# Kernel optimization log

Hardware: AMD Instinct MI355X
Metric: run time of the kernel (lower is better)

The kernel has to match this reference:

```python
import jax, jax.numpy as jnp
import numpy as np

N_HEAD = 16
ROPE_CACHE = 2500  # Rotary module caches tables of length 2500
NEG_INF = -1e30


def _rope_tables(head_dim):
    inv_freq = 1.0 / (10000.0 ** (jnp.arange(0, head_dim, 2, dtype=jnp.float32) / head_dim))
    t = jnp.arange(ROPE_CACHE, dtype=jnp.float32)
    freqs = t[:, None] * inv_freq[None, :]            # (2500, head_dim//2)
    emb = jnp.concatenate([freqs, freqs], axis=-1)    # (2500, head_dim)
    return jnp.cos(emb), jnp.sin(emb)


def _rotate_half(x):
    h = x.shape[-1] // 2
    return jnp.concatenate([-x[..., h:], x[..., :h]], axis=-1)


def setup_inputs() -> dict:
    key = jax.random.key(0)
    ks = jax.random.split(key, 8)
    B, S, D = 2, 2048, 1024
    H = N_HEAD
    hd = D // H
    return {
        "qx": jax.random.normal(ks[0], (B, S, D), jnp.float32),
        "kvx": jax.random.normal(ks[1], (B, S, D), jnp.float32),
        "k_cache": jnp.zeros((B, H, S, hd), jnp.float32),
        "v_cache": jnp.zeros((B, H, S, hd), jnp.float32),
        "Wq": jax.random.normal(ks[2], (D, D), jnp.float32) * 0.02,
        "bq": jnp.zeros((D,), jnp.float32),
        "Wk": jax.random.normal(ks[3], (D, D), jnp.float32) * 0.02,
        "Wv": jax.random.normal(ks[4], (D, D), jnp.float32) * 0.02,
        "bv": jnp.zeros((D,), jnp.float32),
        "Wo": jax.random.normal(ks[5], (D, D), jnp.float32) * 0.02,
        "bo": jnp.zeros((D,), jnp.float32),
        "q_positions": jnp.arange(S, dtype=jnp.int32),
        "kv_positions": jnp.arange(S, dtype=jnp.int32),
    }


def reference(qx, kvx, k_cache, v_cache, Wq, bq, Wk, Wv, bv, Wo, bo, q_positions, kv_positions):
    B, Sq, D = qx.shape
    H = N_HEAD
    hd = D // H
    Skv = kvx.shape[1]
    cos, sin = _rope_tables(hd)
    # sqrt_qk_scale = sqrt(1) = 1, folded out.

    def rope(x, pos):  # x: (B, S, H, hd)
        c = cos[pos][None, :, None, :]
        s = sin[pos][None, :, None, :]
        return x * c + _rotate_half(x) * s

    # projections (torch Linear: y = x @ W.T + b; key has no bias)
    q = (qx @ Wq.T + bq).reshape(B, Sq, H, hd)
    q = rope(q, q_positions).transpose(0, 2, 1, 3)            # (B,H,Sq,hd)
    k = (kvx @ Wk.T).reshape(B, Skv, H, hd)
    k = rope(k, kv_positions).transpose(0, 2, 1, 3)           # (B,H,Skv,hd)
    v = (kvx @ Wv.T + bv).reshape(B, Skv, H, hd).transpose(0, 2, 1, 3)

    # KV-cache scatter update: k_cache[:, :, kv_positions] = k
    k_cache = k_cache.at[:, :, kv_positions].set(k)
    v_cache = v_cache.at[:, :, kv_positions].set(v)
    Sc = k_cache.shape[2]

    # SDPA (causal), scaled by 1/sqrt(head_dim) as in F.scaled_dot_product_attention
    scores = jnp.einsum('bhqd,bhkd->bhqk', q, k_cache) / jnp.sqrt(jnp.float32(hd))
    causal = jnp.arange(Sq)[:, None] >= jnp.arange(Sc)[None, :]
    scores = jnp.where(causal[None, None], scores, NEG_INF)
    attn = jax.nn.softmax(scores, axis=-1)
    wv = jnp.einsum('bhqk,bhkd->bhqd', attn, v_cache)

    out = wv.transpose(0, 2, 1, 3).reshape(B, Sq, D) @ Wo.T + bo
    return out
```

## Files before the change

### kernel.cpp

```cpp
#include <hip/hip_runtime.h>
#include <cstdint>
#include <cstddef>

#define NH   16
#define SEQ  2048
#define DM   1024
#define HD   64
#define KDIM 1024
#define MROWS 4096
#define CH   2

using short8  = __attribute__((ext_vector_type(8))) short;
using short4v = __attribute__((ext_vector_type(4))) short;
using floatx4 = __attribute__((ext_vector_type(4))) float;

__device__ __forceinline__ short f2bf(float f) {
  unsigned int u = __float_as_uint(f);
  u += 0x7fffu + ((u >> 16) & 1u);
  return (short)(u >> 16);
}
__device__ __forceinline__ float bf2f(short s) {
  return __uint_as_float(((unsigned int)(unsigned short)s) << 16);
}
__device__ __forceinline__ unsigned int pktrunc(float lo, float hi) {
  return __builtin_amdgcn_perm(__float_as_uint(hi), __float_as_uint(lo),
                               0x07060302u);
}

__device__ __forceinline__ void async_ld16(const void* g, void* l) {
  __builtin_amdgcn_global_load_lds(
      (const __attribute__((address_space(1))) void*)g,
      (__attribute__((address_space(3))) void*)l, 16, 0, 0);
}

struct Cvt8 {
  const float* src[8];
  void* dst[8];
  int n[8];
  const int* pos[8];
};

__global__ void convert8(Cvt8 a) {
  const int which = blockIdx.y;
  const int stride = gridDim.x * blockDim.x;
  if (which < 6) {
    const float4* s = (const float4*)a.src[which];
    short4v* d = (short4v*)a.dst[which];
    const int n4 = a.n[which] >> 2;
    for (int i = blockIdx.x * blockDim.x + threadIdx.x; i < n4; i += stride) {
      float4 v = s[i];
      short4v o;
      o.x = f2bf(v.x); o.y = f2bf(v.y); o.z = f2bf(v.z); o.w = f2bf(v.w);
      d[i] = o;
    }
  } else {
    const int* pos = a.pos[which];
    float2* d = (float2*)a.dst[which];
    const int n = a.n[which];
    for (int i = blockIdx.x * blockDim.x + threadIdx.x; i < n; i += stride) {
      int s = i >> 5, d1 = i & 31;
      float fr = __powf(10000.f, -(float)d1 * (1.f / 32.f));
      float ang = (float)pos[s] * fr;
      float sn, cs;
      __sincosf(ang, &sn, &cs);
      d[i] = make_float2(cs, sn);
    }
  }
}

__device__ __forceinline__ void gemm_core(const short* __restrict__ A,
                                          const short* __restrict__ B,
                                          int row0, int col0,
                                          short* As, short* Bs,
                                          floatx4 (&acc)[4][4], int tid) {
  const int lane = tid & 63;
  const int w = tid >> 6;
  const int quad = lane >> 4;
  const int ln = lane & 15;
  const int wr = w >> 1, wc = w & 1;
  const int swz = (quad ^ ((ln >> 1) & 3)) * 8;

#pragma unroll
  for (int i = 0; i < 4; ++i)
#pragma unroll
    for (int j = 0; j < 4; ++j) acc[i][j] = (floatx4){0.f, 0.f, 0.f, 0.f};

  for (int k0 = 0; k0 < KDIM; k0 += 64) {
    __syncthreads();
#pragma unroll
    for (int g = 0; g < 4; ++g) {
      int slot = g * 256 + tid;
      int kk = slot >> 9;
      int row = (slot >> 2) & 127;
      int grp = (slot & 3) ^ ((slot >> 3) & 3);
      int src = k0 + kk * 32 + grp * 8;
      async_ld16(A + (size_t)(row0 + row) * KDIM + src, As + slot * 8);
      async_ld16(B + (size_t)(col0 + row) * KDIM + src, Bs + slot * 8);
    }
    __syncthreads();

#pragma unroll
    for (int ks = 0; ks < 2; ++ks) {
      short8 af[4], bfr[4];
#pragma unroll
      for (int i = 0; i < 4; ++i)
        af[i] = *(const short8*)(As + ks * 4096 + (wr * 64 + i * 16 + ln) * 32 + swz);
#pragma unroll
      for (int j = 0; j < 4; ++j)
        bfr[j] = *(const short8*)(Bs + ks * 4096 + (wc * 64 + j * 16 + ln) * 32 + swz);
#pragma unroll
      for (int i = 0; i < 4; ++i)
#pragma unroll
        for (int j = 0; j < 4; ++j)
          acc[i][j] = __builtin_amdgcn_mfma_f32_16x16x32_bf16(af[i], bfr[j], acc[i][j], 0, 0, 0);
    }
  }
}

__global__ __launch_bounds__(256) void proj_gemm(
    const short* __restrict__ qxb, const short* __restrict__ kvxb,
    const short* __restrict__ Wqb, const short* __restrict__ Wkb,
    const short* __restrict__ Wvb,
    const float* __restrict__ bq, const float* __restrict__ bv,
    short* __restrict__ Qo, short* __restrict__ Ko, short* __restrict__ Vt,
    const float2* __restrict__ qtab, const float2* __restrict__ ktab) {
  __shared__ __align__(16) short As[128 * 64];
  __shared__ __align__(16) short Bs[128 * 64];

  const int tid = threadIdx.x;
  const int lane = tid & 63;
  const int w = tid >> 6;
  const int quad = lane >> 4;
  const int ln = lane & 15;
  const int wr = w >> 1, wc = w & 1;
  const int z = blockIdx.z;

  int row0, col0;
  const short *A, *B;
  if (z == 2) {
    A = Wvb; B = kvxb;
    row0 = blockIdx.x * 128;
    col0 = blockIdx.y * 128;
  } else {
    A = z ? kvxb : qxb;
    B = z ? Wkb : Wqb;
    row0 = blockIdx.y * 128;
    col0 = blockIdx.x * 128;
  }

  floatx4 acc[4][4];
  gemm_core(A, B, row0, col0, As, Bs, acc, tid);

  if (z == 2) {
#pragma unroll
    for (int i = 0; i < 4; ++i)
#pragma unroll
      for (int r = 0; r < 4; ++r) {
        int nr = row0 + wr * 64 + i * 16 + quad * 4 + r;
        int h = nr >> 6, d = nr & 63;
        float bb = bv[nr];
        size_t base = ((size_t)(h)*HD + d) * SEQ;
#pragma unroll
        for (int j = 0; j < 4; ++j) {
          int sc = col0 + wc * 64 + j * 16 + ln;
          int b = sc >> 11, s = sc & (SEQ - 1);
          Vt[((size_t)b * NH * HD) * SEQ + base + s] = f2bf(acc[i][j][r] + bb);
        }
      }
  } else {
    const int colbase = col0 + wc * 64;
    const float scale = (z == 0) ? 0.125f : 1.0f;
    const float* bias = (z == 0) ? bq : nullptr;
    const float2* tab = (z == 0) ? qtab : ktab;
    short* Out = (z == 0) ? Qo : Ko;
#pragma unroll
    for (int j = 0; j < 2; ++j) {
      int col1 = colbase + j * 16 + ln;
      float b1 = bias ? bias[col1] : 0.f;
      float b2 = bias ? bias[col1 + 32] : 0.f;
      int h = col1 >> 6;
      int d1 = col1 & 63;
#pragma unroll
      for (int i = 0; i < 4; ++i)
#pragma unroll
        for (int r = 0; r < 4; ++r) {
          int row = row0 + wr * 64 + i * 16 + quad * 4 + r;
          int b = row >> 11, s = row & (SEQ - 1);
          float2 cs_sn = tab[s * 32 + d1];
          float x1 = acc[i][j][r] + b1;
          float x2 = acc[i][j + 2][r] + b2;
          float o1 = (x1 * cs_sn.x - x2 * cs_sn.y) * scale;
          float o2 = (x2 * cs_sn.x + x1 * cs_sn.y) * scale;
          size_t basq = ((((size_t)b * NH + h) * SEQ) + s) * HD;
          Out[basq + d1] = f2bf(o1);
          Out[basq + d1 + 32] = f2bf(o2);
        }
    }
  }
}

__global__ __launch_bounds__(256) void out_gemm(
    const short* __restrict__ Ab, const short* __restrict__ Bb,
    const float* __restrict__ bias, float* __restrict__ out) {
  __shared__ __align__(16) short As[64 * 64];
  __shared__ __align__(16) short Bs[128 * 64];
  const int tid = threadIdx.x;
  const int lane = tid & 63;
  const int w = tid >> 6;
  const int quad = lane >> 4;
  const int ln = lane & 15;
  const int wr = w >> 1, wc = w & 1;
  const int swz = (quad ^ ((ln >> 1) & 3)) * 8;
  const int row0 = (blockIdx.x >> 3) * 64;
  const int col0 = (blockIdx.x & 7) * 128;

  floatx4 acc[2][4];
#pragma unroll
  for (int i = 0; i < 2; ++i)
#pragma unroll
    for (int j = 0; j < 4; ++j) acc[i][j] = (floatx4){0.f, 0.f, 0.f, 0.f};

  for (int k0 = 0; k0 < KDIM; k0 += 64) {
    __syncthreads();
    {
#pragma unroll
      for (int g = 0; g < 2; ++g) {
        int slot = g * 256 + tid;
        int kk = slot >> 8;
        int row = (slot >> 2) & 63;
        int grp = (slot & 3) ^ ((slot >> 3) & 3);
        async_ld16(Ab + (size_t)(row0 + row) * KDIM + k0 + kk * 32 + grp * 8,
                   As + slot * 8);
      }
#pragma unroll
      for (int g = 0; g < 4; ++g) {
        int slot = g * 256 + tid;
        int kk = slot >> 9;
        int row = (slot >> 2) & 127;
        int grp = (slot & 3) ^ ((slot >> 3) & 3);
        async_ld16(Bb + (size_t)(col0 + row) * KDIM + k0 + kk * 32 + grp * 8,
                   Bs + slot * 8);
      }
    }
    __syncthreads();

#pragma unroll
    for (int ks = 0; ks < 2; ++ks) {
      short8 af[2], bfr[4];
#pragma unroll
      for (int i = 0; i < 2; ++i)
        af[i] = *(const short8*)(As + ks * 2048 + (wr * 32 + i * 16 + ln) * 32 + swz);
#pragma unroll
      for (int j = 0; j < 4; ++j)
        bfr[j] = *(const short8*)(Bs + ks * 4096 + (wc * 64 + j * 16 + ln) * 32 + swz);
#pragma unroll
      for (int i = 0; i < 2; ++i)
#pragma unroll
        for (int j = 0; j < 4; ++j)
          acc[i][j] = __builtin_amdgcn_mfma_f32_16x16x32_bf16(af[i], bfr[j], acc[i][j], 0, 0, 0);
    }
  }

#pragma unroll
  for (int j = 0; j < 4; ++j) {
    int col = col0 + wc * 64 + j * 16 + ln;
    float bb = bias[col];
#pragma unroll
    for (int i = 0; i < 2; ++i)
#pragma unroll
      for (int r = 0; r < 4; ++r) {
        int row = row0 + wr * 32 + i * 16 + quad * 4 + r;
        out[(size_t)row * DM + col] = acc[i][j][r] + bb;
      }
  }
}

__global__ __launch_bounds__(256) void attn_partial(
    const short* __restrict__ Q, const short* __restrict__ Kc,
    const short* __restrict__ Vtg, short* __restrict__ Po,
    float* __restrict__ Lo) {
  const int tid = threadIdx.x;
  const int lane = tid & 63;
  const int w = tid >> 6;
  const int quad = lane >> 4;
  const int ln = lane & 15;
  const int swz = (quad ^ ((ln >> 1) & 3)) * 8;
  const int bh = blockIdx.y;
  const int bx = blockIdx.x;
  const int QT = 15 - (bx >> 1);
  const int ch = bx & 1;

  const int q0 = QT * 128;
  const int wlo = q0 + w * 32;

  const short* Qb = Q + (size_t)bh * SEQ * HD;
  const short* Kb = Kc + (size_t)bh * SEQ * HD;
  const short* Vb = Vtg + (size_t)bh * HD * SEQ;

  __shared__ __align__(16) short Ks[2 * 64 * 32];
  __shared__ __align__(16) short Vs[2 * 64 * 32];
  __shared__ __align__(16) short Pt[4][32 * 72];

  short8 qa[2][2];
#pragma unroll
  for (int i = 0; i < 2; ++i)
#pragma unroll
    for (int kk = 0; kk < 2; ++kk)
      qa[i][kk] = *(const short8*)(Qb + (size_t)(wlo + i * 16 + ln) * HD +
                                   quad * 8 + kk * 32);

  floatx4 oacc[4][2];
  float lp[2];
#pragma unroll
  for (int jd = 0; jd < 4; ++jd)
#pragma unroll
    for (int i = 0; i < 2; ++i) oacc[jd][i] = (floatx4){0.f, 0.f, 0.f, 0.f};
  lp[0] = lp[1] = 0.f;

  const int t_end = q0 + 128;
  for (int t = ch * 64; t < t_end; t += CH * 64) {
    __syncthreads();
#pragma unroll
    for (int g = 0; g < 2; ++g) {
      int slot = (w * 2 + g) * 64 + lane;
      int kk = slot >> 8;
      int rowi = (slot >> 2) & 63;
      int grp = (slot & 3) ^ ((slot >> 3) & 3);
      async_ld16(Kb + (size_t)(t + rowi) * HD + kk * 32 + grp * 8,
                 (char*)Ks + slot * 16);
      async_ld16(Vb + (size_t)rowi * SEQ + t + kk * 32 + grp * 8,
                 (char*)Vs + slot * 16);
    }
    __syncthreads();

    if (t > wlo + 31) continue;

    floatx4 sacc[4][2];
#pragma unroll
    for (int c = 0; c < 4; ++c)
#pragma unroll
      for (int i = 0; i < 2; ++i) sacc[c][i] = (floatx4){0.f, 0.f, 0.f, 0.f};
#pragma unroll
    for (int kk = 0; kk < 2; ++kk)
#pragma unroll
      for (int c = 0; c < 4; ++c) {
        short8 kb = *(const short8*)(Ks + kk * 2048 + (c * 16 + ln) * 32 + swz);
        sacc[c][0] = __builtin_amdgcn_mfma_f32_16x16x32_bf16(kb, qa[0][kk], sacc[c][0], 0, 0, 0);
        sacc[c][1] = __builtin_amdgcn_mfma_f32_16x16x32_bf16(kb, qa[1][kk], sacc[c][1], 0, 0, 0);
      }

    const bool dmask = (t + 63 > wlo);
#pragma unroll
    for (int c = 0; c < 4; ++c)
#pragma unroll
      for (int i = 0; i < 2; ++i) {
        float p[4];
#pragma unroll
        for (int r = 0; r < 4; ++r) {
          float pv = __expf(sacc[c][i][r]);
          if (dmask) {
            int sp = t + c * 16 + quad * 4 + r;
            int qq = wlo + i * 16 + ln;
            if (sp > qq) pv = 0.f;
          }
          lp[i] += pv;
          p[r] = pv;
        }
        uint2 uu;
        uu.x = pktrunc(p[0], p[1]);
        uu.y = pktrunc(p[2], p[3]);
        *(uint2*)(&Pt[w][(i * 16 + ln) * 72 + c * 16 + quad * 4]) = uu;
      }

#pragma unroll
    for (int kk = 0; kk < 2; ++kk) {
      short8 pb0 = *(const short8*)(&Pt[w][(ln) * 72 + kk * 32 + quad * 8]);
      short8 pb1 = *(const short8*)(&Pt[w][(16 + ln) * 72 + kk * 32 + quad * 8]);
#pragma unroll
      for (int jd = 0; jd < 4; ++jd) {
        short8 va = *(const short8*)(Vs + kk * 2048 + (jd * 16 + ln) * 32 + swz);
        oacc[jd][0] = __builtin_amdgcn_mfma_f32_16x16x32_bf16(va, pb0, oacc[jd][0], 0, 0, 0);
        oacc[jd][1] = __builtin_amdgcn_mfma_f32_16x16x32_bf16(va, pb1, oacc[jd][1], 0, 0, 0);
      }
    }
  }

  const size_t idx = ((size_t)bh * 16 + QT) * CH + ch;
  short* Pob = Po + idx * 8192;
#pragma unroll
  for (int jd = 0; jd < 4; ++jd)
#pragma unroll
    for (int i = 0; i < 2; ++i) {
      short4v pk;
#pragma unroll
      for (int r = 0; r < 4; ++r) pk[r] = f2bf(oacc[jd][i][r]);
      *(short4v*)(Pob + (w * 32 + i * 16 + ln) * 64 + jd * 16 + quad * 4) = pk;
    }
#pragma unroll
  for (int i = 0; i < 2; ++i) {
    float l = lp[i];
    l += __shfl_xor(l, 16, 64);
    l += __shfl_xor(l, 32, 64);
    if (quad == 0) Lo[idx * 128 + w * 32 + i * 16 + ln] = l;
  }
}

__global__ __launch_bounds__(256) void attn_reduce(
    const short* __restrict__ Po, const float* __restrict__ Lo,
    short* __restrict__ Ov) {
  const int bh = blockIdx.y;
  const int b = bh >> 4, h = bh & 15;
  const int tid = threadIdx.x;
  const int s = blockIdx.x * 64 + (tid >> 2);
  const int d0 = (tid & 3) * 16;
  const int QT = s >> 7, ql = s & 127;
  const size_t i0 = ((size_t)bh * 16 + QT) * CH;

  float l = Lo[i0 * 128 + ql] + Lo[(i0 + 1) * 128 + ql];
  const short8* p0 = (const short8*)(Po + i0 * 8192 + ql * 64 + d0);
  const short8* p1 = (const short8*)(Po + (i0 + 1) * 8192 + ql * 64 + d0);
  short8 a0 = p0[0], a1 = p0[1], c0 = p1[0], c1 = p1[1];
  float inv = 1.f / l;
  short8 o0, o1;
#pragma unroll
  for (int e = 0; e < 8; ++e) {
    o0[e] = f2bf((bf2f(a0[e]) + bf2f(c0[e])) * inv);
    o1[e] = f2bf((bf2f(a1[e]) + bf2f(c1[e])) * inv);
  }
  short* dst = Ov + ((size_t)b * SEQ + s) * DM + h * HD + d0;
  *(short8*)dst = o0;
  *((short8*)dst + 1) = o1;
}

extern "C" void kernel_launch(void* const* d_in, const int* in_sizes, int n_in,
                              void* d_out, int out_size, void* d_ws, size_t ws_size,
                              hipStream_t stream) {
  const float* qx  = (const float*)d_in[0];
  const float* kvx = (const float*)d_in[1];
  const float* Wq = (const float*)d_in[4];
  const float* bq = (const float*)d_in[5];
  const float* Wk = (const float*)d_in[6];
  const float* Wv = (const float*)d_in[7];
  const float* bv = (const float*)d_in[8];
  const float* Wo = (const float*)d_in[9];
  const float* bo = (const float*)d_in[10];
  const int* qpos  = (const int*)d_in[11];
  const int* kvpos = (const int*)d_in[12];

  char* ws = (char*)d_ws;
  short* qxb  = (short*)(ws + 0);
  short* kvxb = (short*)(ws + 8388608);
  short* Wqb  = (short*)(ws + 16777216);
  short* Wkb  = (short*)(ws + 18874368);
  short* Wvb  = (short*)(ws + 20971520);
  short* Wob  = (short*)(ws + 23068672);
  short* Qbf  = (short*)(ws + 25165824);
  short* Kbf  = (short*)(ws + 33554432);
  short* Vtb  = (short*)(ws + 41943040);
  short* WVbf = (short*)(ws + 50331648);
  float2* qtab = (float2*)(ws + 50331648);
  float2* ktab = (float2*)(ws + 50331648 + 524288);
  short* Po = (short*)(ws + 0);
  float* Lo = (float*)(ws + 16777216);

  Cvt8 c;
  c.src[0] = qx;  c.dst[0] = qxb;  c.n[0] = MROWS * KDIM; c.pos[0] = nullptr;
  c.src[1] = kvx; c.dst[1] = kvxb; c.n[1] = MROWS * KDIM; c.pos[1] = nullptr;
  c.src[2] = Wq;  c.dst[2] = Wqb;  c.n[2] = DM * KDIM;    c.pos[2] = nullptr;
  c.src[3] = Wk;  c.dst[3] = Wkb;  c.n[3] = DM * KDIM;    c.pos[3] = nullptr;
  c.src[4] = Wv;  c.dst[4] = Wvb;  c.n[4] = DM * KDIM;    c.pos[4] = nullptr;
  c.src[5] = Wo;  c.dst[5] = Wob;  c.n[5] = DM * KDIM;    c.pos[5] = nullptr;
  c.src[6] = nullptr; c.dst[6] = qtab; c.n[6] = SEQ * 32; c.pos[6] = qpos;
  c.src[7] = nullptr; c.dst[7] = ktab; c.n[7] = SEQ * 32; c.pos[7] = kvpos;
  convert8<<<dim3(1024, 8), 256, 0, stream>>>(c);

  proj_gemm<<<dim3(DM / 128, MROWS / 128, 3), 256, 0, stream>>>(
      qxb, kvxb, Wqb, Wkb, Wvb, bq, bv, Qbf, Kbf, Vtb, qtab, ktab);

  attn_partial<<<dim3(16 * CH, 2 * NH), 256, 0, stream>>>(Qbf, Kbf, Vtb, Po, Lo);

  attn_reduce<<<dim3(SEQ / 64, 2 * NH), 256, 0, stream>>>(Po, Lo, WVbf);

  out_gemm<<<dim3(64 * 8), 256, 0, stream>>>(WVbf, Wob, bo, (float*)d_out);
}
```

Before: 261.3 us.

## Double-buffer shared memory tiles in GEMM and attention kernels

Converts the projection GEMM, output GEMM and attention loops to ping-pong shared-memory buffers. The next tile's async loads are issued before computing on the current one, with a single barrier per iteration. The GEMMs now step K by 32 instead of 64, which halves the work per barrier but hides global-load latency behind MFMA work. Doubled LDS use may reduce occupancy, and the attention Ks/Vs buffers are sized larger than needed.

```diff
diff --git a/kernel.cpp b/kernel.cpp
--- a/kernel.cpp
+++ b/kernel.cpp
@@ -85,35 +85,39 @@
 #pragma unroll
     for (int j = 0; j < 4; ++j) acc[i][j] = (floatx4){0.f, 0.f, 0.f, 0.f};
 
-  for (int k0 = 0; k0 < KDIM; k0 += 64) {
+  auto stage = [&](int k0, int buf) {
+#pragma unroll
+    for (int g = 0; g < 2; ++g) {
+      int slot = g * 256 + tid;
+      int row = slot >> 2;
+      int grp = (slot & 3) ^ ((slot >> 3) & 3);
+      int src = k0 + grp * 8;
+      async_ld16(A + (size_t)(row0 + row) * KDIM + src, As + buf * 4096 + slot * 8);
+      async_ld16(B + (size_t)(col0 + row) * KDIM + src, Bs + buf * 4096 + slot * 8);
+    }
+  };
+
+  stage(0, 0);
+  __syncthreads();
+  int cur = 0;
+  for (int k0 = 0; k0 < KDIM; k0 += 32) {
+    if (k0 + 32 < KDIM) stage(k0 + 32, cur ^ 1);
+    const short* Ab = As + cur * 4096;
+    const short* Bb = Bs + cur * 4096;
+    short8 af[4], bfr[4];
+#pragma unroll
+    for (int i = 0; i < 4; ++i)
+      af[i] = *(const short8*)(Ab + (wr * 64 + i * 16 + ln) * 32 + swz);
+#pragma unroll
+    for (int j = 0; j < 4; ++j)
+      bfr[j] = *(const short8*)(Bb + (wc * 64 + j * 16 + ln) * 32 + swz);
+#pragma unroll
+    for (int i = 0; i < 4; ++i)
+#pragma unroll
+      for (int j = 0; j < 4; ++j)
+        acc[i][j] = __builtin_amdgcn_mfma_f32_16x16x32_bf16(af[i], bfr[j], acc[i][j], 0, 0, 0);
     __syncthreads();
-#pragma unroll
-    for (int g = 0; g < 4; ++g) {
-      int slot = g * 256 + tid;
-      int kk = slot >> 9;
-      int row = (slot >> 2) & 127;
-      int grp = (slot & 3) ^ ((slot >> 3) & 3);
-      int src = k0 + kk * 32 + grp * 8;
-      async_ld16(A + (size_t)(row0 + row) * KDIM + src, As + slot * 8);
-      async_ld16(B + (size_t)(col0 + row) * KDIM + src, Bs + slot * 8);
-    }
-    __syncthreads();
-
-#pragma unroll
-    for (int ks = 0; ks < 2; ++ks) {
-      short8 af[4], bfr[4];
-#pragma unroll
-      for (int i = 0; i < 4; ++i)
-        af[i] = *(const short8*)(As + ks * 4096 + (wr * 64 + i * 16 + ln) * 32 + swz);
-#pragma unroll
-      for (int j = 0; j < 4; ++j)
-        bfr[j] = *(const short8*)(Bs + ks * 4096 + (wc * 64 + j * 16 + ln) * 32 + swz);
-#pragma unroll
-      for (int i = 0; i < 4; ++i)
-#pragma unroll
-        for (int j = 0; j < 4; ++j)
-          acc[i][j] = __builtin_amdgcn_mfma_f32_16x16x32_bf16(af[i], bfr[j], acc[i][j], 0, 0, 0);
-    }
+    cur ^= 1;
   }
 }
 
@@ -124,8 +128,8 @@
     const float* __restrict__ bq, const float* __restrict__ bv,
     short* __restrict__ Qo, short* __restrict__ Ko, short* __restrict__ Vt,
     const float2* __restrict__ qtab, const float2* __restrict__ ktab) {
-  __shared__ __align__(16) short As[128 * 64];
-  __shared__ __align__(16) short Bs[128 * 64];
+  __shared__ __align__(16) short As[2 * 4096];
+  __shared__ __align__(16) short Bs[2 * 4096];
 
   const int tid = threadIdx.x;
   const int lane = tid & 63;
@@ -202,8 +206,8 @@
 __global__ __launch_bounds__(256) void out_gemm(
     const short* __restrict__ Ab, const short* __restrict__ Bb,
     const float* __restrict__ bias, float* __restrict__ out) {
-  __shared__ __align__(16) short As[64 * 64];
-  __shared__ __align__(16) short Bs[128 * 64];
+  __shared__ __align__(16) short As[2 * 2048];
+  __shared__ __align__(16) short Bs[2 * 4096];
   const int tid = threadIdx.x;
   const int lane = tid & 63;
   const int w = tid >> 6;
@@ -220,45 +224,45 @@
 #pragma unroll
     for (int j = 0; j < 4; ++j) acc[i][j] = (floatx4){0.f, 0.f, 0.f, 0.f};
 
-  for (int k0 = 0; k0 < KDIM; k0 += 64) {
+  auto stage = [&](int k0, int buf) {
+    {
+      int slot = tid;
+      int row = slot >> 2;
+      int grp = (slot & 3) ^ ((slot >> 3) & 3);
+      async_ld16(Ab + (size_t)(row0 + row) * KDIM + k0 + grp * 8,
+                 As + buf * 2048 + slot * 8);
+    }
+#pragma unroll
+    for (int g = 0; g < 2; ++g) {
+      int slot = g * 256 + tid;
+      int row = slot >> 2;
+      int grp = (slot & 3) ^ ((slot >> 3) & 3);
+      async_ld16(Bb + (size_t)(col0 + row) * KDIM + k0 + grp * 8,
+                 Bs + buf * 4096 + slot * 8);
+    }
+  };
+
+  stage(0, 0);
+  __syncthreads();
+  int cur = 0;
+  for (int k0 = 0; k0 < KDIM; k0 += 32) {
+    if (k0 + 32 < KDIM) stage(k0 + 32, cur ^ 1);
+    const short* Ac = As + cur * 2048;
+    const short* Bc = Bs + cur * 4096;
+    short8 af[2], bfr[4];
+#pragma unroll
+    for (int i = 0; i < 2; ++i)
+      af[i] = *(const short8*)(Ac + (wr * 32 + i * 16 + ln) * 32 + swz);
+#pragma unroll
+    for (int j = 0; j < 4; ++j)
+      bfr[j] = *(const short8*)(Bc + (wc * 64 + j * 16 + ln) * 32 + swz);
+#pragma unroll
+    for (int i = 0; i < 2; ++i)
+#pragma unroll
+      for (int j = 0; j < 4; ++j)
+        acc[i][j] = __builtin_amdgcn_mfma_f32_16x16x32_bf16(af[i], bfr[j], acc[i][j], 0, 0, 0);
     __syncthreads();
-    {
-#pragma unroll
-      for (int g = 0; g < 2; ++g) {
-        int slot = g * 256 + tid;
-        int kk = slot >> 8;
-        int row = (slot >> 2) & 63;
-        int grp = (slot & 3) ^ ((slot >> 3) & 3);
-        async_ld16(Ab + (size_t)(row0 + row) * KDIM + k0 + kk * 32 + grp * 8,
-                   As + slot * 8);
-      }
-#pragma unroll
-      for (int g = 0; g < 4; ++g) {
-        int slot = g * 256 + tid;
-        int kk = slot >> 9;
-        int row = (slot >> 2) & 127;
-        int grp = (slot & 3) ^ ((slot >> 3) & 3);
-        async_ld16(Bb + (size_t)(col0 + row) * KDIM + k0 + kk * 32 + grp * 8,
-                   Bs + slot * 8);
-      }
-    }
-    __syncthreads();
-
-#pragma unroll
-    for (int ks = 0; ks < 2; ++ks) {
-      short8 af[2], bfr[4];
-#pragma unroll
-      for (int i = 0; i < 2; ++i)
-        af[i] = *(const short8*)(As + ks * 2048 + (wr * 32 + i * 16 + ln) * 32 + swz);
-#pragma unroll
-      for (int j = 0; j < 4; ++j)
-        bfr[j] = *(const short8*)(Bs + ks * 4096 + (wc * 64 + j * 16 + ln) * 32 + swz);
-#pragma unroll
-      for (int i = 0; i < 2; ++i)
-#pragma unroll
-        for (int j = 0; j < 4; ++j)
-          acc[i][j] = __builtin_amdgcn_mfma_f32_16x16x32_bf16(af[i], bfr[j], acc[i][j], 0, 0, 0);
-    }
+    cur ^= 1;
   }
 
 #pragma unroll
@@ -297,8 +301,8 @@
   const short* Kb = Kc + (size_t)bh * SEQ * HD;
   const short* Vb = Vtg + (size_t)bh * HD * SEQ;
 
-  __shared__ __align__(16) short Ks[2 * 64 * 32];
-  __shared__ __align__(16) short Vs[2 * 64 * 32];
+  __shared__ __align__(16) short Ks[2 * 4096];
+  __shared__ __align__(16) short Vs[2 * 4096];
   __shared__ __align__(16) short Pt[4][32 * 72];
 
   short8 qa[2][2];
@@ -317,9 +321,7 @@
     for (int i = 0; i < 2; ++i) oacc[jd][i] = (floatx4){0.f, 0.f, 0.f, 0.f};
   lp[0] = lp[1] = 0.f;
 
-  const int t_end = q0 + 128;
-  for (int t = ch * 64; t < t_end; t += CH * 64) {
-    __syncthreads();
+  auto stage = [&](int t, int buf) {
 #pragma unroll
     for (int g = 0; g < 2; ++g) {
       int slot = (w * 2 + g) * 64 + lane;
@@ -327,62 +329,74 @@
       int rowi = (slot >> 2) & 63;
       int grp = (slot & 3) ^ ((slot >> 3) & 3);
       async_ld16(Kb + (size_t)(t + rowi) * HD + kk * 32 + grp * 8,
-                 (char*)Ks + slot * 16);
+                 Ks + buf * 4096 + slot * 8);
       async_ld16(Vb + (size_t)rowi * SEQ + t + kk * 32 + grp * 8,
-                 (char*)Vs + slot * 16);
+                 Vs + buf * 4096 + slot * 8);
+    }
+  };
+
+  const int t_end = q0 + 128;
+  const int t0 = ch * 64;
+  stage(t0, 0);
+  __syncthreads();
+  int cur = 0;
+  for (int t = t0; t < t_end; t += CH * 64) {
+    if (t + CH * 64 < t_end) stage(t + CH * 64, cur ^ 1);
+
+    if (t <= wlo + 31) {
+      const short* Kcur = Ks + cur * 4096;
+      const short* Vcur = Vs + cur * 4096;
+      floatx4 sacc[4][2];
+#pragma unroll
+      for (int c = 0; c < 4; ++c)
+#pragma unroll
+        for (int i = 0; i < 2; ++i) sacc[c][i] = (floatx4){0.f, 0.f, 0.f, 0.f};
+#pragma unroll
+      for (int kk = 0; kk < 2; ++kk)
+#pragma unroll
+        for (int c = 0; c < 4; ++c) {
+          short8 kb = *(const short8*)(Kcur + kk * 2048 + (c * 16 + ln) * 32 + swz);
+          sacc[c][0] = __builtin_amdgcn_mfma_f32_16x16x32_bf16(kb, qa[0][kk], sacc[c][0], 0, 0, 0);
+          sacc[c][1] = __builtin_amdgcn_mfma_f32_16x16x32_bf16(kb, qa[1][kk], sacc[c][1], 0, 0, 0);
+        }
+
+      const bool dmask = (t + 63 > wlo);
+#pragma unroll
+      for (int c = 0; c < 4; ++c)
+#pragma unroll
+        for (int i = 0; i < 2; ++i) {
+          float p[4];
+#pragma unroll
+          for (int r = 0; r < 4; ++r) {
+            float pv = __expf(sacc[c][i][r]);
+            if (dmask) {
+              int sp = t + c * 16 + quad * 4 + r;
+              int qq = wlo + i * 16 + ln;
+              if (sp > qq) pv = 0.f;
+            }
+            lp[i] += pv;
+            p[r] = pv;
+          }
+          uint2 uu;
+          uu.x = pktrunc(p[0], p[1]);
+          uu.y = pktrunc(p[2], p[3]);
+          *(uint2*)(&Pt[w][(i * 16 + ln) * 72 + c * 16 + quad * 4]) = uu;
+        }
+
+#pragma unroll
+      for (int kk = 0; kk < 2; ++kk) {
+        short8 pb0 = *(const short8*)(&Pt[w][(ln) * 72 + kk * 32 + quad * 8]);
+        short8 pb1 = *(const short8*)(&Pt[w][(16 + ln) * 72 + kk * 32 + quad * 8]);
+#pragma unroll
+        for (int jd = 0; jd < 4; ++jd) {
+          short8 va = *(const short8*)(Vcur + kk * 2048 + (jd * 16 + ln) * 32 + swz);
+          oacc[jd][0] = __builtin_amdgcn_mfma_f32_16x16x32_bf16(va, pb0, oacc[jd][0], 0, 0, 0);
+          oacc[jd][1] = __builtin_amdgcn_mfma_f32_16x16x32_bf16(va, pb1, oacc[jd][1], 0, 0, 0);
+        }
+      }
     }
     __syncthreads();
-
-    if (t > wlo + 31) continue;
-
-    floatx4 sacc[4][2];
-#pragma unroll
-    for (int c = 0; c < 4; ++c)
-#pragma unroll
-      for (int i = 0; i < 2; ++i) sacc[c][i] = (floatx4){0.f, 0.f, 0.f, 0.f};
-#pragma unroll
-    for (int kk = 0; kk < 2; ++kk)
-#pragma unroll
-      for (int c = 0; c < 4; ++c) {
-        short8 kb = *(const short8*)(Ks + kk * 2048 + (c * 16 + ln) * 32 + swz);
-        sacc[c][0] = __builtin_amdgcn_mfma_f32_16x16x32_bf16(kb, qa[0][kk], sacc[c][0], 0, 0, 0);
-        sacc[c][1] = __builtin_amdgcn_mfma_f32_16x16x32_bf16(kb, qa[1][kk], sacc[c][1], 0, 0, 0);
-      }
-
-    const bool dmask = (t + 63 > wlo);
-#pragma unroll
-    for (int c = 0; c < 4; ++c)
-#pragma unroll
-      for (int i = 0; i < 2; ++i) {
-        float p[4];
-#pragma unroll
-        for (int r = 0; r < 4; ++r) {
-          float pv = __expf(sacc[c][i][r]);
-          if (dmask) {
-            int sp = t + c * 16 + quad * 4 + r;
-            int qq = wlo + i * 16 + ln;
-            if (sp > qq) pv = 0.f;
-          }
-          lp[i] += pv;
-          p[r] = pv;
-        }
-        uint2 uu;
-        uu.x = pktrunc(p[0], p[1]);
-        uu.y = pktrunc(p[2], p[3]);
-        *(uint2*)(&Pt[w][(i * 16 + ln) * 72 + c * 16 + quad * 4]) = uu;
-      }
-
-#pragma unroll
-    for (int kk = 0; kk < 2; ++kk) {
-      short8 pb0 = *(const short8*)(&Pt[w][(ln) * 72 + kk * 32 + quad * 8]);
-      short8 pb1 = *(const short8*)(&Pt[w][(16 + ln) * 72 + kk * 32 + quad * 8]);
-#pragma unroll
-      for (int jd = 0; jd < 4; ++jd) {
-        short8 va = *(const short8*)(Vs + kk * 2048 + (jd * 16 + ln) * 32 + swz);
-        oacc[jd][0] = __builtin_amdgcn_mfma_f32_16x16x32_bf16(va, pb0, oacc[jd][0], 0, 0, 0);
-        oacc[jd][1] = __builtin_amdgcn_mfma_f32_16x16x32_bf16(va, pb1, oacc[jd][1], 0, 0, 0);
-      }
-    }
+    cur ^= 1;
   }
 
   const size_t idx = ((size_t)bh * 16 + QT) * CH + ch;
```

Result: slower. 275.2 us (+5.3%).
